# Kernel tuning notes

Measured on AMD Instinct MI355X. Metric: run time of the kernel, lower is better.

Reference implementation:

```python
import math
import jax, jax.numpy as jnp
import numpy as np


def setup_inputs() -> dict:
    key = jax.random.key(0)
    k1, k2 = jax.random.split(key)
    B, Sq, Sk, H, Hkv, D = 2, 2048, 2048, 16, 8, 128
    q = jax.random.normal(k1, (B, Sq, H, D), dtype=jnp.float32)
    kv = jax.random.normal(k2, (B, Sk, 2, Hkv, D), dtype=jnp.float32)
    return {"q": q, "kv": kv}


def reference(q, kv):
    # q: [B, Sq, H, D]; kv: [B, Sk, 2, Hkv, D]
    B, Sq, H, D = q.shape
    Sk = kv.shape[1]
    Hkv = kv.shape[3]
    if Hkv != H:
        # GQA: repeat each kv head g times consecutively ('... hkv d -> ... (hkv g) d')
        kv = jnp.repeat(kv, H // Hkv, axis=3)
    k = kv[:, :, 0]  # [B, Sk, H, D]
    v = kv[:, :, 1]  # [B, Sk, H, D]
    q = q.astype(jnp.float32)
    k = k.astype(jnp.float32)
    scale = 1.0 / math.sqrt(D)
    # scores: [B, H, Sq, Sk]
    scores = jnp.einsum('bqhd,bkhd->bhqk', q, k * scale)
    # causal mask with right-alignment offset: mask where col > row + Sk - Sq
    rows = jnp.arange(Sq)[:, None]
    cols = jnp.arange(Sk)[None, :]
    causal_mask = cols > rows + (Sk - Sq)  # [Sq, Sk]
    scores = jnp.where(causal_mask[None, None], jnp.float32(-10000.0), scores)
    attention = jax.nn.softmax(scores, axis=-1).astype(v.dtype)
    # output: [B, Sq, H, D]
    out = jnp.einsum('bhqk,bkhd->bqhd', attention, v)
    return out
```

## Files before the change

### kernel.cpp

```cpp
#include <hip/hip_runtime.h>
#include <stdint.h>


#define SQ 2048
#define SK 2048
#define NH 16
#define NKV 8
#define DH 128
#define KVSTRIDE (2*NKV*DH)
#define SCALE_LOG2E 0.12751743f

typedef __attribute__((ext_vector_type(8))) short bf8;
typedef __attribute__((ext_vector_type(4))) float f4;

__device__ __forceinline__ float fast_exp2(float x) {
  return __builtin_amdgcn_exp2f(x);
}

__device__ __forceinline__ short f2bf(float f) {
  uint32_t u = __builtin_bit_cast(uint32_t, f);
  u += 0x7FFFu + ((u >> 16) & 1u);
  return (short)(u >> 16);
}

__device__ __forceinline__ bf8 pack8(f4 a, f4 b) {
  bf8 v;
  v[0] = f2bf(a[0]); v[1] = f2bf(a[1]); v[2] = f2bf(a[2]); v[3] = f2bf(a[3]);
  v[4] = f2bf(b[0]); v[5] = f2bf(b[1]); v[6] = f2bf(b[2]); v[7] = f2bf(b[3]);
  return v;
}
__device__ __forceinline__ bf8 pack8s(f4 a, f4 b, float s) {
  bf8 v;
  v[0] = f2bf(a[0]*s); v[1] = f2bf(a[1]*s); v[2] = f2bf(a[2]*s); v[3] = f2bf(a[3]*s);
  v[4] = f2bf(b[0]*s); v[5] = f2bf(b[1]*s); v[6] = f2bf(b[2]*s); v[7] = f2bf(b[3]*s);
  return v;
}

template<int CTRL>
__device__ __forceinline__ float dppmov(float x) {
  int xi = __builtin_bit_cast(int, x);
  int r = __builtin_amdgcn_update_dpp(xi, xi, CTRL, 0xF, 0xF, false);
  return __builtin_bit_cast(float, r);
}
__device__ __forceinline__ float rowsum16(float v) {
  v += dppmov<0x121>(v);
  v += dppmov<0x122>(v);
  v += dppmov<0x124>(v);
  v += dppmov<0x128>(v);
  return v;
}
__device__ __forceinline__ float rowmax16(float v) {
  v = fmaxf(v, dppmov<0x121>(v));
  v = fmaxf(v, dppmov<0x122>(v));
  v = fmaxf(v, dppmov<0x124>(v));
  v = fmaxf(v, dppmov<0x128>(v));
  return v;
}

__device__ __forceinline__ void g2l16(const short* g, short* l) {
  __builtin_amdgcn_global_load_lds(
      (const __attribute__((address_space(1))) uint32_t*)g,
      (__attribute__((address_space(3))) uint32_t*)l, 16, 0, 0);
}

__global__ void conv_kv(const float* __restrict__ kv,
                        short* __restrict__ Kb, short* __restrict__ Vb) {
  int id = blockIdx.x * 256 + threadIdx.x;
  if (blockIdx.y == 0) {
    int c   = id & 15;
    int key = (id >> 4) & 63;
    int kt  = (id >> 10) & 31;
    int hk  = (id >> 15) & 7;
    int b   = (id >> 18) & 1;
    const float* src = kv + ((size_t)(b * SK + kt * 64 + key) * 2) * (NKV * DH)
                          + hk * DH + c * 8;
    f4 a = *(const f4*)src;
    f4 bb = *(const f4*)(src + 4);
    short* dst = Kb + ((size_t)((b * 8 + hk) * 32 + kt)) * 8192;
    *(bf8*)&dst[(key * 16 + (c ^ (key & 7))) * 8] = pack8(a, bb);
  } else {
    int d  = id & 127;
    int c  = (id >> 7) & 7;
    int kt = (id >> 10) & 31;
    int hk = (id >> 15) & 7;
    int b  = (id >> 18) & 1;
    const float* src = kv + ((size_t)(b * SK + kt * 64 + c * 8) * 2 + 1) * (NKV * DH)
                          + hk * DH + d;
    bf8 v;
#pragma unroll
    for (int kk = 0; kk < 8; ++kk) v[kk] = f2bf(src[(size_t)kk * KVSTRIDE]);
    short* dst = Vb + ((size_t)((b * 8 + hk) * 32 + kt)) * 8192;
    *(bf8*)&dst[(d * 8 + (c ^ (d & 7))) * 8] = v;
  }
}

__launch_bounds__(256, 2)
__global__ void fa_fwd4(const float* __restrict__ q,
                        const short* __restrict__ Kb,
                        const short* __restrict__ Vb,
                        float* __restrict__ out) {
  __shared__ __align__(16) short lsK[2][8192];
  __shared__ __align__(16) short lsV[2][8192];
  __shared__ __align__(16) short lsP[4][1024];

  const int tid  = threadIdx.x;
  const int w    = tid >> 6;
  const int l    = tid & 63;
  const int l15  = l & 15;
  const int quad = l >> 4;

  const int bx  = blockIdx.x;
  const int s   = bx >> 4;
  const int qt  = (s < 16) ? (31 - s) : (s - 16);
  const int bhk = bx & 15;
  const int b   = bhk >> 3;
  const int hk  = bhk & 7;
  const int head  = hk * 2 + (w & 1);
  const int mrow0 = (w >> 1) * 32;
  const int q0    = qt * 64;

  const short* ktiles = Kb + ((size_t)((b * 8 + hk) * 32)) * 8192;
  const short* vtiles = Vb + ((size_t)((b * 8 + hk) * 32)) * 8192;
  short* myP = lsP[w];

  auto stage = [&](int kt, int nb) {
    const short* ks = ktiles + (size_t)kt * 8192 + tid * 8;
    const short* vs = vtiles + (size_t)kt * 8192 + tid * 8;
#pragma unroll
    for (int i = 0; i < 4; ++i) {
      g2l16(ks + i * 2048, &lsK[nb][i * 2048 + tid * 8]);
      g2l16(vs + i * 2048, &lsV[nb][i * 2048 + tid * 8]);
    }
  };

  bf8 qf[2][4];
#pragma unroll
  for (int mt = 0; mt < 2; ++mt) {
    int row = q0 + mrow0 + mt * 16 + l15;
    const float* qr = q + ((size_t)(b * SQ + row) * NH + head) * DH;
#pragma unroll
    for (int kc = 0; kc < 4; ++kc) {
      const float* src = qr + kc * 32 + quad * 8;
      f4 a = *(const f4*)src;
      f4 c = *(const f4*)(src + 4);
      qf[mt][kc] = pack8s(a, c, SCALE_LOG2E);
    }
  }

  f4 O[2][8];
#pragma unroll
  for (int mt = 0; mt < 2; ++mt)
#pragma unroll
    for (int nt = 0; nt < 8; ++nt) O[mt][nt] = (f4){0.f, 0.f, 0.f, 0.f};
  float lpart[2][4] = {{0.f, 0.f, 0.f, 0.f}, {0.f, 0.f, 0.f, 0.f}};

  stage(0, 0);

#pragma unroll 1
  for (int kt = 0; kt <= qt; ++kt) {
    const int cur = kt & 1;
    __syncthreads();
    if (kt < qt) stage(kt + 1, cur ^ 1);

    f4 S[2][4];
#pragma unroll
    for (int mt = 0; mt < 2; ++mt)
#pragma unroll
      for (int nt = 0; nt < 4; ++nt) S[mt][nt] = (f4){0.f, 0.f, 0.f, 0.f};
    __builtin_amdgcn_s_setprio(1);
#pragma unroll
    for (int kc = 0; kc < 4; ++kc) {
#pragma unroll
      for (int nt = 0; nt < 4; ++nt) {
        int key = nt * 16 + l15;
        int c   = kc * 4 + quad;
        bf8 kf = *(const bf8*)&lsK[cur][(key * 16 + (c ^ (key & 7))) * 8];
        S[0][nt] = __builtin_amdgcn_mfma_f32_16x16x32_bf16(qf[0][kc], kf, S[0][nt], 0, 0, 0);
        S[1][nt] = __builtin_amdgcn_mfma_f32_16x16x32_bf16(qf[1][kc], kf, S[1][nt], 0, 0, 0);
      }
    }
    __builtin_amdgcn_s_setprio(0);

    if (kt == qt) {
#pragma unroll
      for (int mt = 0; mt < 2; ++mt)
#pragma unroll
        for (int nt = 0; nt < 4; ++nt)
#pragma unroll
          for (int r = 0; r < 4; ++r) {
            int rloc = mrow0 + mt * 16 + quad * 4 + r;
            int kloc = nt * 16 + l15;
            if (kloc > rloc) S[mt][nt][r] = -1e30f;
          }
    }

#pragma unroll
    for (int kc = 0; kc < 2; ++kc) {
#pragma unroll
      for (int mt = 0; mt < 2; ++mt)
#pragma unroll
        for (int ntl = 0; ntl < 2; ++ntl) {
          int nt = kc * 2 + ntl;
#pragma unroll
          for (int r = 0; r < 4; ++r) {
            float pe = fast_exp2(S[mt][nt][r]);
            lpart[mt][r] += pe;
            int m  = mt * 16 + quad * 4 + r;
            int kk = ntl * 16 + l15;
            myP[(m * 4 + ((kk >> 3) ^ ((m >> 2) & 3))) * 8 + (kk & 7)] = f2bf(pe);
          }
        }

      bf8 pf[2];
#pragma unroll
      for (int mt = 0; mt < 2; ++mt) {
        int m = mt * 16 + l15;
        pf[mt] = *(const bf8*)&myP[(m * 4 + (quad ^ ((m >> 2) & 3))) * 8];
      }
      __builtin_amdgcn_s_setprio(1);
#pragma unroll
      for (int nt = 0; nt < 8; ++nt) {
        int d = nt * 16 + l15;
        int c = kc * 4 + quad;
        bf8 vf = *(const bf8*)&lsV[cur][(d * 8 + (c ^ (d & 7))) * 8];
        O[0][nt] = __builtin_amdgcn_mfma_f32_16x16x32_bf16(pf[0], vf, O[0][nt], 0, 0, 0);
        O[1][nt] = __builtin_amdgcn_mfma_f32_16x16x32_bf16(pf[1], vf, O[1][nt], 0, 0, 0);
      }
      __builtin_amdgcn_s_setprio(0);
    }
  }

#pragma unroll
  for (int mt = 0; mt < 2; ++mt)
#pragma unroll
    for (int r = 0; r < 4; ++r) {
      float linv = 1.0f / rowsum16(lpart[mt][r]);
      int row = q0 + mrow0 + mt * 16 + quad * 4 + r;
      float* dst = out + ((size_t)(b * SQ + row) * NH + head) * DH + l15;
#pragma unroll
      for (int nt = 0; nt < 8; ++nt) dst[nt * 16] = O[mt][nt][r] * linv;
    }
}

__launch_bounds__(256, 2)
__global__ void fa_fwd_v1(const float* __restrict__ q,
                          const float* __restrict__ kv,
                          float* __restrict__ out) {
  __shared__ __align__(16) short lsK[64 * 128];
  __shared__ __align__(16) short lsV[128 * 64];
  __shared__ __align__(16) short lsP[4][32 * 64];

  const int tid  = threadIdx.x;
  const int w    = tid >> 6;
  const int l    = tid & 63;
  const int l15  = l & 15;
  const int quad = l >> 4;

  const int bx  = blockIdx.x;
  const int qt  = 31 - (bx >> 4);
  const int bhk = bx & 15;
  const int b   = bhk >> 3;
  const int hk  = bhk & 7;
  const int head  = hk * 2 + (w >> 1);
  const int mrow0 = (w & 1) * 32;
  const int q0    = qt * 64;

  const float* kbase = kv + (size_t)b * SK * KVSTRIDE + (size_t)hk * DH;
  const float* vbase = kbase + NKV * DH;

  bf8 qf[2][4];
#pragma unroll
  for (int mt = 0; mt < 2; ++mt)
#pragma unroll
    for (int kc = 0; kc < 4; ++kc) {
      int row = q0 + mrow0 + mt * 16 + l15;
      int d0  = kc * 32 + quad * 8;
      const float* src = q + ((size_t)(b * SQ + row) * NH + head) * DH + d0;
      f4 a = *(const f4*)src;
      f4 c = *(const f4*)(src + 4);
      qf[mt][kc] = pack8s(a, c, SCALE_LOG2E);
    }

  f4 O[2][8];
  float mrow[2][4], lrow[2][4];
#pragma unroll
  for (int mt = 0; mt < 2; ++mt) {
#pragma unroll
    for (int nt = 0; nt < 8; ++nt) O[mt][nt] = (f4){0.f, 0.f, 0.f, 0.f};
#pragma unroll
    for (int r = 0; r < 4; ++r) { mrow[mt][r] = -1e30f; lrow[mt][r] = 0.f; }
  }

  for (int kt = 0; kt <= qt; ++kt) {
    if (kt) __syncthreads();
    const int k0 = kt * 64;
#pragma unroll
    for (int i = 0; i < 4; ++i) {
      int id  = i * 256 + tid;
      int key = id >> 4;
      int c   = id & 15;
      const float* src = kbase + (size_t)(k0 + key) * KVSTRIDE + c * 8;
      f4 a = *(const f4*)src;
      f4 bb = *(const f4*)(src + 4);
      *(bf8*)&lsK[(key * 16 + (c ^ (key & 7))) * 8] = pack8(a, bb);
    }
#pragma unroll
    for (int i = 0; i < 4; ++i) {
      int u  = i * 4 + w;
      int kg = u >> 1;
      int d  = (u & 1) * 64 + l;
      const float* src = vbase + (size_t)(k0 + kg * 8) * KVSTRIDE + d;
      bf8 v;
#pragma unroll
      for (int kk = 0; kk < 8; ++kk) v[kk] = f2bf(src[(size_t)kk * KVSTRIDE]);
      *(bf8*)&lsV[(d * 8 + (kg ^ (d & 7))) * 8] = v;
    }
    __syncthreads();

    f4 S[2][4];
#pragma unroll
    for (int mt = 0; mt < 2; ++mt)
#pragma unroll
      for (int nt = 0; nt < 4; ++nt) S[mt][nt] = (f4){0.f, 0.f, 0.f, 0.f};
#pragma unroll
    for (int kc = 0; kc < 4; ++kc)
#pragma unroll
      for (int nt = 0; nt < 4; ++nt) {
        int key = nt * 16 + l15;
        int c   = kc * 4 + quad;
        bf8 kf = *(const bf8*)&lsK[(key * 16 + (c ^ (key & 7))) * 8];
        S[0][nt] = __builtin_amdgcn_mfma_f32_16x16x32_bf16(qf[0][kc], kf, S[0][nt], 0, 0, 0);
        S[1][nt] = __builtin_amdgcn_mfma_f32_16x16x32_bf16(qf[1][kc], kf, S[1][nt], 0, 0, 0);
      }

    if (kt == qt) {
#pragma unroll
      for (int mt = 0; mt < 2; ++mt)
#pragma unroll
        for (int nt = 0; nt < 4; ++nt)
#pragma unroll
          for (int r = 0; r < 4; ++r) {
            int rloc = mrow0 + mt * 16 + quad * 4 + r;
            int kloc = nt * 16 + l15;
            if (kloc > rloc) S[mt][nt][r] = -1e30f;
          }
    }

#pragma unroll
    for (int mt = 0; mt < 2; ++mt)
#pragma unroll
      for (int r = 0; r < 4; ++r) {
        float mx = fmaxf(fmaxf(S[mt][0][r], S[mt][1][r]),
                         fmaxf(S[mt][2][r], S[mt][3][r]));
        mx = rowmax16(mx);
        float mold = mrow[mt][r];
        float mnew = fmaxf(mold, mx);
        float alpha = fast_exp2(mold - mnew);
        mrow[mt][r] = mnew;
        float rs = 0.f;
#pragma unroll
        for (int nt = 0; nt < 4; ++nt) {
          float pe = fast_exp2(S[mt][nt][r] - mnew);
          S[mt][nt][r] = pe;
          rs += pe;
        }
        rs = rowsum16(rs);
        lrow[mt][r] = lrow[mt][r] * alpha + rs;
#pragma unroll
        for (int nt = 0; nt < 8; ++nt) O[mt][nt][r] *= alpha;
        int m = mt * 16 + quad * 4 + r;
#pragma unroll
        for (int nt = 0; nt < 4; ++nt) {
          int key = nt * 16 + l15;
          lsP[w][(m * 8 + ((key >> 3) ^ (m & 7))) * 8 + (key & 7)] =
              f2bf(S[mt][nt][r]);
        }
      }

#pragma unroll
    for (int kc = 0; kc < 2; ++kc) {
      bf8 pf[2];
#pragma unroll
      for (int mt = 0; mt < 2; ++mt) {
        int m = mt * 16 + l15;
        int c = kc * 4 + quad;
        pf[mt] = *(const bf8*)&lsP[w][(m * 8 + (c ^ (m & 7))) * 8];
      }
#pragma unroll
      for (int nt = 0; nt < 8; ++nt) {
        int d = nt * 16 + l15;
        int c = kc * 4 + quad;
        bf8 vf = *(const bf8*)&lsV[(d * 8 + (c ^ (d & 7))) * 8];
        O[0][nt] = __builtin_amdgcn_mfma_f32_16x16x32_bf16(pf[0], vf, O[0][nt], 0, 0, 0);
        O[1][nt] = __builtin_amdgcn_mfma_f32_16x16x32_bf16(pf[1], vf, O[1][nt], 0, 0, 0);
      }
    }
  }

#pragma unroll
  for (int mt = 0; mt < 2; ++mt)
#pragma unroll
    for (int r = 0; r < 4; ++r) {
      float linv = 1.0f / lrow[mt][r];
      int row = q0 + mrow0 + mt * 16 + quad * 4 + r;
      float* dst = out + ((size_t)(b * SQ + row) * NH + head) * DH + l15;
#pragma unroll
      for (int nt = 0; nt < 8; ++nt) dst[nt * 16] = O[mt][nt][r] * linv;
    }
}

extern "C" void kernel_launch(void* const* d_in, const int* in_sizes, int n_in,
                              void* d_out, int out_size, void* d_ws, size_t ws_size,
                              hipStream_t stream) {
  const float* q  = (const float*)d_in[0];
  const float* kv = (const float*)d_in[1];
  float* out      = (float*)d_out;
  (void)in_sizes; (void)n_in; (void)out_size;

  const size_t kb_elems = (size_t)2 * 8 * 32 * 8192;
  const size_t need = 2 * kb_elems * sizeof(short);

  if (ws_size >= need) {
    short* Kb = (short*)d_ws;
    short* Vb = Kb + kb_elems;
    conv_kv<<<dim3(2048, 2), 256, 0, stream>>>(kv, Kb, Vb);
    fa_fwd4<<<dim3(512), dim3(256), 0, stream>>>(q, Kb, Vb, out);
  } else {
    fa_fwd_v1<<<dim3(512), dim3(256), 0, stream>>>(q, kv, out);
  }
}
```

Before: 161.5 us.

## Rewrite attention kernel with 512-thread blocks, key-split waves, and paired causal tiles

Replaces the 256-thread kernel with a 512-thread version in which two wave groups each handle half of every 64-key tile, and their partial outputs and row sums are reduced through shared memory at the end. Each block now handles a pair of query tiles (p and 31-p) in sequence so causal work is balanced across blocks, and the grid is halved. Scores are computed as K·Q so the probability accumulators can be packed directly into MFMA operand registers with v_cvt_pk_bf16_f32, which removes the LDS round trip for P. The K layout in the conversion kernel is permuted to match. The risks are the extra reduction and barriers, fewer resident blocks, and the correctness of the permuted key masking.

```diff
diff --git a/kernel.cpp b/kernel.cpp
--- a/kernel.cpp
+++ b/kernel.cpp
@@ -12,6 +12,7 @@
 
 typedef __attribute__((ext_vector_type(8))) short bf8;
 typedef __attribute__((ext_vector_type(4))) float f4;
+typedef __attribute__((ext_vector_type(4))) int i4;
 
 __device__ __forceinline__ float fast_exp2(float x) {
   return __builtin_amdgcn_exp2f(x);
@@ -21,6 +22,12 @@
   uint32_t u = __builtin_bit_cast(uint32_t, f);
   u += 0x7FFFu + ((u >> 16) & 1u);
   return (short)(u >> 16);
+}
+
+__device__ __forceinline__ int cvtpk(float lo, float hi) {
+  int r;
+  asm("v_cvt_pk_bf16_f32 %0, %1, %2" : "=v"(r) : "v"(lo), "v"(hi));
+  return r;
 }
 
 __device__ __forceinline__ bf8 pack8(f4 a, f4 b) {
@@ -77,7 +84,8 @@
     f4 a = *(const f4*)src;
     f4 bb = *(const f4*)(src + 4);
     short* dst = Kb + ((size_t)((b * 8 + hk) * 32 + kt)) * 8192;
-    *(bf8*)&dst[(key * 16 + (c ^ (key & 7))) * 8] = pack8(a, bb);
+    int akey = (key & 0x23) | ((key & 4) << 2) | ((key & 0x18) >> 1);
+    *(bf8*)&dst[(akey * 16 + (c ^ (akey & 7))) * 8] = pack8(a, bb);
   } else {
     int d  = id & 127;
     int c  = (id >> 7) & 7;
@@ -94,14 +102,13 @@
   }
 }
 
-__launch_bounds__(256, 2)
-__global__ void fa_fwd4(const float* __restrict__ q,
+__launch_bounds__(512, 2)
+__global__ void fa_fwd6(const float* __restrict__ q,
                         const short* __restrict__ Kb,
                         const short* __restrict__ Vb,
                         float* __restrict__ out) {
-  __shared__ __align__(16) short lsK[2][8192];
-  __shared__ __align__(16) short lsV[2][8192];
-  __shared__ __align__(16) short lsP[4][1024];
+  __shared__ __align__(16) short lsKV[4][8192];
+  __shared__ __align__(16) short lsPad[12288];
 
   const int tid  = threadIdx.x;
   const int w    = tid >> 6;
@@ -110,136 +117,171 @@
   const int quad = l >> 4;
 
   const int bx  = blockIdx.x;
-  const int s   = bx >> 4;
-  const int qt  = (s < 16) ? (31 - s) : (s - 16);
+  const int p   = bx >> 4;
   const int bhk = bx & 15;
   const int b   = bhk >> 3;
   const int hk  = bhk & 7;
+
+  const int h     = w >> 2;
   const int head  = hk * 2 + (w & 1);
-  const int mrow0 = (w >> 1) * 32;
-  const int q0    = qt * 64;
+  const int mrow0 = ((w >> 1) & 1) * 32;
 
   const short* ktiles = Kb + ((size_t)((b * 8 + hk) * 32)) * 8192;
   const short* vtiles = Vb + ((size_t)((b * 8 + hk) * 32)) * 8192;
-  short* myP = lsP[w];
 
   auto stage = [&](int kt, int nb) {
     const short* ks = ktiles + (size_t)kt * 8192 + tid * 8;
     const short* vs = vtiles + (size_t)kt * 8192 + tid * 8;
 #pragma unroll
-    for (int i = 0; i < 4; ++i) {
-      g2l16(ks + i * 2048, &lsK[nb][i * 2048 + tid * 8]);
-      g2l16(vs + i * 2048, &lsV[nb][i * 2048 + tid * 8]);
+    for (int i = 0; i < 2; ++i) {
+      g2l16(ks + i * 4096, &lsKV[nb][i * 4096 + tid * 8]);
+      g2l16(vs + i * 4096, &lsKV[2 + nb][i * 4096 + tid * 8]);
     }
   };
 
-  bf8 qf[2][4];
-#pragma unroll
-  for (int mt = 0; mt < 2; ++mt) {
-    int row = q0 + mrow0 + mt * 16 + l15;
-    const float* qr = q + ((size_t)(b * SQ + row) * NH + head) * DH;
-#pragma unroll
-    for (int kc = 0; kc < 4; ++kc) {
-      const float* src = qr + kc * 32 + quad * 8;
-      f4 a = *(const f4*)src;
-      f4 c = *(const f4*)(src + 4);
-      qf[mt][kc] = pack8s(a, c, SCALE_LOG2E);
-    }
-  }
-
-  f4 O[2][8];
-#pragma unroll
-  for (int mt = 0; mt < 2; ++mt)
-#pragma unroll
-    for (int nt = 0; nt < 8; ++nt) O[mt][nt] = (f4){0.f, 0.f, 0.f, 0.f};
-  float lpart[2][4] = {{0.f, 0.f, 0.f, 0.f}, {0.f, 0.f, 0.f, 0.f}};
-
-  stage(0, 0);
-
 #pragma unroll 1
-  for (int kt = 0; kt <= qt; ++kt) {
-    const int cur = kt & 1;
-    __syncthreads();
-    if (kt < qt) stage(kt + 1, cur ^ 1);
-
-    f4 S[2][4];
+  for (int phase = 0; phase < 2; ++phase) {
+    const int qt = phase ? (31 - p) : p;
+    const int q0 = qt * 64;
+
+    bf8 qf[2][4];
+#pragma unroll
+    for (int mt = 0; mt < 2; ++mt) {
+      int row = q0 + mrow0 + mt * 16 + l15;
+      const float* qr = q + ((size_t)(b * SQ + row) * NH + head) * DH;
+#pragma unroll
+      for (int kc = 0; kc < 4; ++kc) {
+        const float* src = qr + kc * 32 + quad * 8;
+        f4 a = *(const f4*)src;
+        f4 c = *(const f4*)(src + 4);
+        qf[mt][kc] = pack8s(a, c, SCALE_LOG2E);
+      }
+    }
+
+    f4 O[2][8];
 #pragma unroll
     for (int mt = 0; mt < 2; ++mt)
 #pragma unroll
-      for (int nt = 0; nt < 4; ++nt) S[mt][nt] = (f4){0.f, 0.f, 0.f, 0.f};
-    __builtin_amdgcn_s_setprio(1);
-#pragma unroll
-    for (int kc = 0; kc < 4; ++kc) {
-#pragma unroll
-      for (int nt = 0; nt < 4; ++nt) {
-        int key = nt * 16 + l15;
-        int c   = kc * 4 + quad;
-        bf8 kf = *(const bf8*)&lsK[cur][(key * 16 + (c ^ (key & 7))) * 8];
-        S[0][nt] = __builtin_amdgcn_mfma_f32_16x16x32_bf16(qf[0][kc], kf, S[0][nt], 0, 0, 0);
-        S[1][nt] = __builtin_amdgcn_mfma_f32_16x16x32_bf16(qf[1][kc], kf, S[1][nt], 0, 0, 0);
-      }
-    }
-    __builtin_amdgcn_s_setprio(0);
-
-    if (kt == qt) {
+      for (int nt = 0; nt < 8; ++nt) O[mt][nt] = (f4){0.f, 0.f, 0.f, 0.f};
+    float lpart[2] = {0.f, 0.f};
+
+    if (phase) __syncthreads();
+    stage(0, 0);
+
+    for (int kt = 0; kt <= qt; ++kt) {
+      const int cur = kt & 1;
+      __syncthreads();
+      if (kt < qt) stage(kt + 1, cur ^ 1);
+
+      f4 S[2][2];
 #pragma unroll
       for (int mt = 0; mt < 2; ++mt)
 #pragma unroll
-        for (int nt = 0; nt < 4; ++nt)
-#pragma unroll
-          for (int r = 0; r < 4; ++r) {
-            int rloc = mrow0 + mt * 16 + quad * 4 + r;
-            int kloc = nt * 16 + l15;
-            if (kloc > rloc) S[mt][nt][r] = -1e30f;
-          }
-    }
-
-#pragma unroll
-    for (int kc = 0; kc < 2; ++kc) {
+        for (int nt = 0; nt < 2; ++nt) S[mt][nt] = (f4){0.f, 0.f, 0.f, 0.f};
+#pragma unroll
+      for (int kc = 0; kc < 4; ++kc) {
+#pragma unroll
+        for (int nt = 0; nt < 2; ++nt) {
+          int row = h * 32 + nt * 16 + l15;
+          int c   = kc * 4 + quad;
+          bf8 kf = *(const bf8*)&lsKV[cur][(row * 16 + (c ^ (row & 7))) * 8];
+          S[0][nt] = __builtin_amdgcn_mfma_f32_16x16x32_bf16(kf, qf[0][kc], S[0][nt], 0, 0, 0);
+          S[1][nt] = __builtin_amdgcn_mfma_f32_16x16x32_bf16(kf, qf[1][kc], S[1][nt], 0, 0, 0);
+        }
+      }
+
+      if (kt == qt) {
+#pragma unroll
+        for (int mt = 0; mt < 2; ++mt)
+#pragma unroll
+          for (int nt = 0; nt < 2; ++nt)
+#pragma unroll
+            for (int r = 0; r < 4; ++r) {
+              int kphys = h * 32 + (quad << 3) + (nt << 2) + r;
+              if (kphys > mrow0 + mt * 16 + l15) S[mt][nt][r] = -1e30f;
+            }
+      }
+
 #pragma unroll
       for (int mt = 0; mt < 2; ++mt)
 #pragma unroll
-        for (int ntl = 0; ntl < 2; ++ntl) {
-          int nt = kc * 2 + ntl;
+        for (int nt = 0; nt < 2; ++nt)
 #pragma unroll
           for (int r = 0; r < 4; ++r) {
             float pe = fast_exp2(S[mt][nt][r]);
-            lpart[mt][r] += pe;
-            int m  = mt * 16 + quad * 4 + r;
-            int kk = ntl * 16 + l15;
-            myP[(m * 4 + ((kk >> 3) ^ ((m >> 2) & 3))) * 8 + (kk & 7)] = f2bf(pe);
+            S[mt][nt][r] = pe;
+            lpart[mt] += pe;
           }
-        }
 
       bf8 pf[2];
 #pragma unroll
       for (int mt = 0; mt < 2; ++mt) {
-        int m = mt * 16 + l15;
-        pf[mt] = *(const bf8*)&myP[(m * 4 + (quad ^ ((m >> 2) & 3))) * 8];
-      }
-      __builtin_amdgcn_s_setprio(1);
+        i4 wv;
+        wv[0] = cvtpk(S[mt][0][0], S[mt][0][1]);
+        wv[1] = cvtpk(S[mt][0][2], S[mt][0][3]);
+        wv[2] = cvtpk(S[mt][1][0], S[mt][1][1]);
+        wv[3] = cvtpk(S[mt][1][2], S[mt][1][3]);
+        pf[mt] = __builtin_bit_cast(bf8, wv);
+      }
+
 #pragma unroll
       for (int nt = 0; nt < 8; ++nt) {
         int d = nt * 16 + l15;
-        int c = kc * 4 + quad;
-        bf8 vf = *(const bf8*)&lsV[cur][(d * 8 + (c ^ (d & 7))) * 8];
+        int c = h * 4 + quad;
+        bf8 vf = *(const bf8*)&lsKV[2 + cur][(d * 8 + (c ^ (d & 7))) * 8];
         O[0][nt] = __builtin_amdgcn_mfma_f32_16x16x32_bf16(pf[0], vf, O[0][nt], 0, 0, 0);
         O[1][nt] = __builtin_amdgcn_mfma_f32_16x16x32_bf16(pf[1], vf, O[1][nt], 0, 0, 0);
       }
-      __builtin_amdgcn_s_setprio(0);
+    }
+
+    __syncthreads();
+    if (w >= 4) {
+      int uw = w - 4;
+      float* base = (float*)lsKV[uw] + (size_t)l * 64;
+#pragma unroll
+      for (int mt = 0; mt < 2; ++mt)
+#pragma unroll
+        for (int nt = 0; nt < 8; ++nt) {
+          int t    = mt * 8 + nt;
+          int slot = (t + l15) & 15;
+          *(f4*)(base + slot * 4) = O[mt][nt];
+        }
+      float* lp = (float*)lsPad;
+      lp[(uw * 64 + l) * 2 + 0] = lpart[0];
+      lp[(uw * 64 + l) * 2 + 1] = lpart[1];
+    }
+    __syncthreads();
+    if (w < 4) {
+      float* base = (float*)lsKV[w] + (size_t)l * 64;
+#pragma unroll
+      for (int mt = 0; mt < 2; ++mt)
+#pragma unroll
+        for (int nt = 0; nt < 8; ++nt) {
+          int t    = mt * 8 + nt;
+          int slot = (t + l15) & 15;
+          O[mt][nt] += *(const f4*)(base + slot * 4);
+        }
+      const float* lp = (const float*)lsPad;
+      lpart[0] += lp[(w * 64 + l) * 2 + 0];
+      lpart[1] += lp[(w * 64 + l) * 2 + 1];
+
+#pragma unroll
+      for (int mt = 0; mt < 2; ++mt) {
+        float lsum = lpart[mt];
+        lsum += __shfl_xor(lsum, 16);
+        lsum += __shfl_xor(lsum, 32);
+#pragma unroll
+        for (int r = 0; r < 4; ++r) {
+          float lr   = __shfl(lsum, quad * 4 + r);
+          float linv = 1.0f / lr;
+          int row = q0 + mrow0 + mt * 16 + quad * 4 + r;
+          float* dst = out + ((size_t)(b * SQ + row) * NH + head) * DH + l15;
+#pragma unroll
+          for (int nt = 0; nt < 8; ++nt) dst[nt * 16] = O[mt][nt][r] * linv;
+        }
+      }
     }
   }
-
-#pragma unroll
-  for (int mt = 0; mt < 2; ++mt)
-#pragma unroll
-    for (int r = 0; r < 4; ++r) {
-      float linv = 1.0f / rowsum16(lpart[mt][r]);
-      int row = q0 + mrow0 + mt * 16 + quad * 4 + r;
-      float* dst = out + ((size_t)(b * SQ + row) * NH + head) * DH + l15;
-#pragma unroll
-      for (int nt = 0; nt < 8; ++nt) dst[nt * 16] = O[mt][nt][r] * linv;
-    }
 }
 
 __launch_bounds__(256, 2)
@@ -424,7 +466,7 @@
     short* Kb = (short*)d_ws;
     short* Vb = Kb + kb_elems;
     conv_kv<<<dim3(2048, 2), 256, 0, stream>>>(kv, Kb, Vb);
-    fa_fwd4<<<dim3(512), dim3(256), 0, stream>>>(q, Kb, Vb, out);
+    fa_fwd6<<<dim3(256), dim3(512), 0, stream>>>(q, Kb, Vb, out);
   } else {
     fa_fwd_v1<<<dim3(512), dim3(256), 0, stream>>>(q, kv, out);
   }
```

New measurement: 148.1 us. -8.2%, faster.
